# Kernel tuning notes

Measured on AMD Instinct MI355X. Metric: run time of the kernel, lower is better.

Reference implementation:

```python
import jax, jax.numpy as jnp
import numpy as np

LN_EPS = 1e-5


def setup_inputs() -> dict:
    key = jax.random.key(0)
    kA, kX, kh = jax.random.split(key, 3)
    B, N, Cin, C, K = 16, 1024, 64, 64, 3
    A = jax.random.normal(kA, (B, N, N), dtype=jnp.float32)
    X = jax.random.normal(kX, (B, N, Cin), dtype=jnp.float32)
    h = jax.random.normal(kh, (K + 1, C, N), dtype=jnp.float32)
    ln_gamma = jnp.ones((C,), dtype=jnp.float32)
    ln_beta = jnp.zeros((C,), dtype=jnp.float32)
    return {"A": A, "X": X, "h": h, "ln_gamma": ln_gamma, "ln_beta": ln_beta}


def reference(A, X, h, ln_gamma, ln_beta):
    # Original loops compute, for each output channel c:
    #   sum_i sum_ch diag(h[i,c]) @ A^i @ X[..., ch]
    # which equals sum_i h[i,c,:] * (A^i @ X.sum(-1)).
    num_terms = h.shape[0] - 1  # static
    Xs = X.sum(-1)  # [B, N]
    powers = [Xs]
    p = Xs
    for _ in range(num_terms):  # static small loop over polynomial terms
        p = jnp.einsum('bnm,bm->bn', A, p)  # A^i @ Xs, matrix-vector per batch
        powers.append(p)
    P = jnp.stack(powers)  # [K+1, B, N]
    # node-variant per-channel taps: Y[b,n,c] = sum_i h[i,c,n] * P[i,b,n]
    Y = jnp.einsum('icn,ibn->bnc', h, P)  # [B, N, C]
    mu = Y.mean(axis=-1, keepdims=True)
    var = Y.var(axis=-1, keepdims=True)
    Yn = (Y - mu) / jnp.sqrt(var + LN_EPS) * ln_gamma + ln_beta
    return jnp.tanh(Yn)
```

## Files before the change

kernel.cpp:

```cpp
#include <hip/hip_runtime.h>
#include <math.h>

constexpr int B = 16, N = 1024, Cin = 64, C = 64, K = 3;
#define LN_EPS 1e-5f

__global__ void __launch_bounds__(256) k_sumx(const float* __restrict__ X,
                                              float* __restrict__ P0) {
    int wave = (blockIdx.x * blockDim.x + threadIdx.x) >> 6;
    int lane = threadIdx.x & 63;
    float v = X[(size_t)wave * Cin + lane];
    #pragma unroll
    for (int off = 32; off; off >>= 1) v += __shfl_xor(v, off);
    if (lane == 0) P0[wave] = v;
}

__global__ void __launch_bounds__(256) k_transpose_h(const float* __restrict__ h,
                                                     float* __restrict__ ht) {
    __shared__ float tile[64][65];
    int i  = blockIdx.x / (N / 64);
    int n0 = (blockIdx.x % (N / 64)) * 64;
    int tx = threadIdx.x & 63;
    int ty = threadIdx.x >> 6;
    const float* hi = h + (size_t)i * C * N;
    #pragma unroll
    for (int cc = ty; cc < 64; cc += 4)
        tile[cc][tx] = hi[(size_t)cc * N + n0 + tx];
    __syncthreads();
    float* hti = ht + (size_t)i * N * C;
    #pragma unroll
    for (int nn = ty; nn < 64; nn += 4)
        hti[(size_t)(n0 + nn) * C + tx] = tile[tx][nn];
}

__global__ void __launch_bounds__(256) k_matvec(const float* __restrict__ A,
                                                const float* __restrict__ x,
                                                float* __restrict__ y) {
    __shared__ float4 xs[N / 4];
    int b    = blockIdx.x >> 6;
    int row0 = (blockIdx.x & 63) << 4;
    const float4* xv = (const float4*)(x + (size_t)b * N);
    xs[threadIdx.x] = xv[threadIdx.x];
    __syncthreads();

    int w    = threadIdx.x >> 6;
    int lane = threadIdx.x & 63;
    int row  = row0 + w * 4;
    const float* Ab = A + ((size_t)b << 20);
    const float4* r0 = (const float4*)(Ab + (size_t)(row + 0) * N);
    const float4* r1 = (const float4*)(Ab + (size_t)(row + 1) * N);
    const float4* r2 = (const float4*)(Ab + (size_t)(row + 2) * N);
    const float4* r3 = (const float4*)(Ab + (size_t)(row + 3) * N);

    float a0 = 0.f, a1 = 0.f, a2 = 0.f, a3 = 0.f;
    #pragma unroll
    for (int k = 0; k < 4; ++k) {
        int idx = k * 64 + lane;
        float4 xx = xs[idx];
        float4 v0 = r0[idx];
        float4 v1 = r1[idx];
        float4 v2 = r2[idx];
        float4 v3 = r3[idx];
        a0 += v0.x * xx.x + v0.y * xx.y + v0.z * xx.z + v0.w * xx.w;
        a1 += v1.x * xx.x + v1.y * xx.y + v1.z * xx.z + v1.w * xx.w;
        a2 += v2.x * xx.x + v2.y * xx.y + v2.z * xx.z + v2.w * xx.w;
        a3 += v3.x * xx.x + v3.y * xx.y + v3.z * xx.z + v3.w * xx.w;
    }
    #pragma unroll
    for (int off = 32; off; off >>= 1) {
        a0 += __shfl_xor(a0, off);
        a1 += __shfl_xor(a1, off);
        a2 += __shfl_xor(a2, off);
        a3 += __shfl_xor(a3, off);
    }
    if (lane == 0) {
        float* yb = y + (size_t)b * N + row;
        yb[0] = a0; yb[1] = a1; yb[2] = a2; yb[3] = a3;
    }
}

__global__ void __launch_bounds__(256) k_epilogue(const float* __restrict__ P,
                                                  const float* __restrict__ ht,
                                                  const float* __restrict__ gamma,
                                                  const float* __restrict__ beta,
                                                  float* __restrict__ out) {
    int wave = (blockIdx.x * blockDim.x + threadIdx.x) >> 6;
    int lane = threadIdx.x & 63;
    int b = wave >> 10;
    int n = wave & 1023;

    float y = 0.f;
    #pragma unroll
    for (int i = 0; i <= K; ++i) {
        float hv = ht[((size_t)i * N + n) * C + lane];
        float pv = P[((size_t)i * B + b) * N + n];
        y += hv * pv;
    }
    float s = y;
    #pragma unroll
    for (int off = 32; off; off >>= 1) s += __shfl_xor(s, off);
    float mu = s * (1.0f / 64.0f);
    float d = y - mu;
    float v = d * d;
    #pragma unroll
    for (int off = 32; off; off >>= 1) v += __shfl_xor(v, off);
    float var = v * (1.0f / 64.0f);
    float yn = d * rsqrtf(var + LN_EPS) * gamma[lane] + beta[lane];
    out[(size_t)wave * C + lane] = tanhf(yn);
}

extern "C" void kernel_launch(void* const* d_in, const int* in_sizes, int n_in,
                              void* d_out, int out_size, void* d_ws, size_t ws_size,
                              hipStream_t stream) {
    const float* A     = (const float*)d_in[0];
    const float* X     = (const float*)d_in[1];
    const float* h     = (const float*)d_in[2];
    const float* gamma = (const float*)d_in[3];
    const float* beta  = (const float*)d_in[4];
    float* out = (float*)d_out;

    float* P  = (float*)d_ws;
    float* ht = P + (size_t)(K + 1) * B * N;

    k_sumx<<<B * N / 4, 256, 0, stream>>>(X, P);
    k_transpose_h<<<(K + 1) * (N / 64), 256, 0, stream>>>(h, ht);
    for (int i = 0; i < K; ++i)
        k_matvec<<<B * (N / 16), 256, 0, stream>>>(A, P + (size_t)i * B * N,
                                                   P + (size_t)(i + 1) * B * N);
    k_epilogue<<<B * N / 4, 256, 0, stream>>>(P, ht, gamma, beta, out);
}
```

Baseline: 138.4 us.

## Fuse X-sum with h transpose and fold final matvec into LayerNorm epilogue

```diff
diff --git a/kernel.cpp b/kernel.cpp
--- a/kernel.cpp
+++ b/kernel.cpp
@@ -4,54 +4,47 @@
 constexpr int B = 16, N = 1024, Cin = 64, C = 64, K = 3;
 #define LN_EPS 1e-5f
 
-__global__ void __launch_bounds__(256) k_sumx(const float* __restrict__ X,
-                                              float* __restrict__ P0) {
-    int wave = (blockIdx.x * blockDim.x + threadIdx.x) >> 6;
-    int lane = threadIdx.x & 63;
-    float v = X[(size_t)wave * Cin + lane];
-    #pragma unroll
-    for (int off = 32; off; off >>= 1) v += __shfl_xor(v, off);
-    if (lane == 0) P0[wave] = v;
+__global__ void __launch_bounds__(256) k_front(const float* __restrict__ X,
+                                               const float* __restrict__ h,
+                                               float* __restrict__ P,
+                                               float* __restrict__ ht) {
+    __shared__ float tile[64 * 65];
+    const int tid  = threadIdx.x;
+    const int lane = tid & 63;
+    const int w    = tid >> 6;
+    const int gw   = blockIdx.x * 4 + w;
+
+    for (int p = gw; p < B * N; p += 4096) {
+        float v = X[(size_t)p * Cin + lane];
+        #pragma unroll
+        for (int off = 32; off; off >>= 1) v += __shfl_xor(v, off);
+        if (lane == 0) P[p] = v;
+    }
+
+    if (blockIdx.x < (K + 1) * (N / 64)) {
+        int i  = blockIdx.x / (N / 64);
+        int n0 = (blockIdx.x % (N / 64)) * 64;
+        const float* hi = h + (size_t)i * C * N;
+        #pragma unroll
+        for (int cc = w; cc < 64; cc += 4)
+            tile[cc * 65 + lane] = hi[(size_t)cc * N + n0 + lane];
+        __syncthreads();
+        float* hti = ht + (size_t)i * N * C;
+        #pragma unroll
+        for (int nn = w; nn < 64; nn += 4)
+            hti[(size_t)(n0 + nn) * C + lane] = tile[lane * 65 + nn];
+    }
 }
 
-__global__ void __launch_bounds__(256) k_transpose_h(const float* __restrict__ h,
-                                                     float* __restrict__ ht) {
-    __shared__ float tile[64][65];
-    int i  = blockIdx.x / (N / 64);
-    int n0 = (blockIdx.x % (N / 64)) * 64;
-    int tx = threadIdx.x & 63;
-    int ty = threadIdx.x >> 6;
-    const float* hi = h + (size_t)i * C * N;
-    #pragma unroll
-    for (int cc = ty; cc < 64; cc += 4)
-        tile[cc][tx] = hi[(size_t)cc * N + n0 + tx];
-    __syncthreads();
-    float* hti = ht + (size_t)i * N * C;
-    #pragma unroll
-    for (int nn = ty; nn < 64; nn += 4)
-        hti[(size_t)(n0 + nn) * C + tx] = tile[tx][nn];
-}
-
-__global__ void __launch_bounds__(256) k_matvec(const float* __restrict__ A,
-                                                const float* __restrict__ x,
-                                                float* __restrict__ y) {
-    __shared__ float4 xs[N / 4];
-    int b    = blockIdx.x >> 6;
-    int row0 = (blockIdx.x & 63) << 4;
-    const float4* xv = (const float4*)(x + (size_t)b * N);
-    xs[threadIdx.x] = xv[threadIdx.x];
-    __syncthreads();
-
-    int w    = threadIdx.x >> 6;
-    int lane = threadIdx.x & 63;
-    int row  = row0 + w * 4;
-    const float* Ab = A + ((size_t)b << 20);
+__device__ __forceinline__ void matvec4(const float* __restrict__ Ab,
+                                        const float4* __restrict__ xs,
+                                        int row, int lane,
+                                        float& a0, float& a1, float& a2, float& a3) {
     const float4* r0 = (const float4*)(Ab + (size_t)(row + 0) * N);
     const float4* r1 = (const float4*)(Ab + (size_t)(row + 1) * N);
     const float4* r2 = (const float4*)(Ab + (size_t)(row + 2) * N);
     const float4* r3 = (const float4*)(Ab + (size_t)(row + 3) * N);
-
-    float a0 = 0.f, a1 = 0.f, a2 = 0.f, a3 = 0.f;
+    a0 = a1 = a2 = a3 = 0.f;
     #pragma unroll
     for (int k = 0; k < 4; ++k) {
         int idx = k * 64 + lane;
@@ -72,40 +65,77 @@
         a2 += __shfl_xor(a2, off);
         a3 += __shfl_xor(a3, off);
     }
+}
+
+__global__ void __launch_bounds__(256) k_matvec(const float* __restrict__ A,
+                                                const float* __restrict__ x,
+                                                float* __restrict__ y) {
+    __shared__ __align__(16) float4 xs[N / 4];
+    const int b    = blockIdx.x >> 6;
+    const int row0 = (blockIdx.x & 63) << 4;
+    xs[threadIdx.x] = ((const float4*)(x + (size_t)b * N))[threadIdx.x];
+    __syncthreads();
+
+    const int w    = threadIdx.x >> 6;
+    const int lane = threadIdx.x & 63;
+    float a0, a1, a2, a3;
+    matvec4(A + ((size_t)b << 20), xs, row0 + w * 4, lane, a0, a1, a2, a3);
     if (lane == 0) {
-        float* yb = y + (size_t)b * N + row;
+        float* yb = y + (size_t)b * N + row0 + w * 4;
         yb[0] = a0; yb[1] = a1; yb[2] = a2; yb[3] = a3;
     }
 }
 
-__global__ void __launch_bounds__(256) k_epilogue(const float* __restrict__ P,
-                                                  const float* __restrict__ ht,
-                                                  const float* __restrict__ gamma,
-                                                  const float* __restrict__ beta,
-                                                  float* __restrict__ out) {
-    int wave = (blockIdx.x * blockDim.x + threadIdx.x) >> 6;
-    int lane = threadIdx.x & 63;
-    int b = wave >> 10;
-    int n = wave & 1023;
+__global__ void __launch_bounds__(256) k_last(const float* __restrict__ A,
+                                              const float* __restrict__ P,
+                                              const float* __restrict__ ht,
+                                              const float* __restrict__ gamma,
+                                              const float* __restrict__ beta,
+                                              float* __restrict__ out) {
+    __shared__ __align__(16) float4 xs[N / 4];
+    __shared__ float p3s[16];
+    const int b    = blockIdx.x >> 6;
+    const int row0 = (blockIdx.x & 63) << 4;
+    const float* x2 = P + (size_t)2 * B * N + (size_t)b * N;
+    xs[threadIdx.x] = ((const float4*)x2)[threadIdx.x];
+    __syncthreads();
 
-    float y = 0.f;
+    const int w    = threadIdx.x >> 6;
+    const int lane = threadIdx.x & 63;
+    float a0, a1, a2, a3;
+    matvec4(A + ((size_t)b << 20), xs, row0 + w * 4, lane, a0, a1, a2, a3);
+    if (lane == 0) {
+        p3s[w * 4 + 0] = a0; p3s[w * 4 + 1] = a1;
+        p3s[w * 4 + 2] = a2; p3s[w * 4 + 3] = a3;
+    }
+    __syncthreads();
+
+    const float g = gamma[lane];
+    const float be = beta[lane];
     #pragma unroll
-    for (int i = 0; i <= K; ++i) {
-        float hv = ht[((size_t)i * N + n) * C + lane];
-        float pv = P[((size_t)i * B + b) * N + n];
-        y += hv * pv;
+    for (int j = 0; j < 4; ++j) {
+        const int nn = w * 4 + j;
+        const int n  = row0 + nn;
+        float y = 0.f;
+        #pragma unroll
+        for (int i = 0; i < 3; ++i) {
+            float hv = ht[((size_t)i * N + n) * C + lane];
+            float pv = P[(size_t)i * B * N + (size_t)b * N + n];
+            y += hv * pv;
+        }
+        y += ht[((size_t)3 * N + n) * C + lane] * p3s[nn];
+        float s = y;
+        #pragma unroll
+        for (int off = 32; off; off >>= 1) s += __shfl_xor(s, off);
+        float mu = s * (1.0f / 64.0f);
+        float d  = y - mu;
+        float v  = d * d;
+        #pragma unroll
+        for (int off = 32; off; off >>= 1) v += __shfl_xor(v, off);
+        float var = v * (1.0f / 64.0f);
+        float yn  = d * rsqrtf(var + LN_EPS) * g + be;
+        out[((size_t)b * N + n) * C + lane] = tanhf(yn);
     }
-    float s = y;
-    #pragma unroll
-    for (int off = 32; off; off >>= 1) s += __shfl_xor(s, off);
-    float mu = s * (1.0f / 64.0f);
-    float d = y - mu;
-    float v = d * d;
-    #pragma unroll
-    for (int off = 32; off; off >>= 1) v += __shfl_xor(v, off);
-    float var = v * (1.0f / 64.0f);
-    float yn = d * rsqrtf(var + LN_EPS) * gamma[lane] + beta[lane];
-    out[(size_t)wave * C + lane] = tanhf(yn);
 }
 
 extern "C" void kernel_launch(void* const* d_in, const int* in_sizes, int n_in,
@@ -119,12 +149,11 @@
     float* out = (float*)d_out;
 
     float* P  = (float*)d_ws;
-    float* ht = P + (size_t)(K + 1) * B * N;
+    float* ht = P + (size_t)3 * B * N;
 
-    k_sumx<<<B * N / 4, 256, 0, stream>>>(X, P);
-    k_transpose_h<<<(K + 1) * (N / 64), 256, 0, stream>>>(h, ht);
-    for (int i = 0; i < K; ++i)
-        k_matvec<<<B * (N / 16), 256, 0, stream>>>(A, P + (size_t)i * B * N,
-                                                   P + (size_t)(i + 1) * B * N);
-    k_epilogue<<<B * N / 4, 256, 0, stream>>>(P, ht, gamma, beta, out);
+    k_front<<<1024, 256, 0, stream>>>(X, h, P, ht);
+    k_matvec<<<B * (N / 16), 256, 0, stream>>>(A, P, P + (size_t)B * N);
+    k_matvec<<<B * (N / 16), 256, 0, stream>>>(A, P + (size_t)B * N,
+                                               P + (size_t)2 * B * N);
+    k_last<<<B * (N / 16), 256, 0, stream>>>(A, P, ht, gamma, beta, out);
 }
```

Result: no change. 136.6 us (-1.3%).
